# Optimization experiments

Measured on AMD Instinct MI355X. Metric: run time of the kernel, lower is better.

Reference implementation:

```python
import jax, jax.numpy as jnp
import numpy as np

D_MODEL = 768
N_HEADS = 12
HEAD_DIM = D_MODEL // N_HEADS


def setup_inputs() -> dict:
    key = jax.random.key(0)
    k_x, k_wqkv, k_bqkv, k_wp, k_bp = jax.random.split(key, 5)
    s = 1.0 / np.sqrt(D_MODEL)
    return {
        "x": jax.random.normal(k_x, (8, 1024, D_MODEL), dtype=jnp.float32),
        "w_qkv": jax.random.uniform(k_wqkv, (D_MODEL, 3 * D_MODEL), jnp.float32, -s, s),
        "b_qkv": jax.random.uniform(k_bqkv, (3 * D_MODEL,), jnp.float32, -s, s),
        "w_proj": jax.random.uniform(k_wp, (D_MODEL, D_MODEL), jnp.float32, -s, s),
        "b_proj": jax.random.uniform(k_bp, (D_MODEL,), jnp.float32, -s, s),
    }


def reference(x, w_qkv, b_qkv, w_proj, b_proj):
    # x: [B, N, D]. Dropout is identity in eval mode.
    B, N, D = x.shape
    qkv = x @ w_qkv + b_qkv  # [B, N, 3D]
    qkv = qkv.reshape(B, N, 3, N_HEADS, HEAD_DIM).transpose(2, 0, 3, 1, 4)
    q, k, v = qkv[0], qkv[1], qkv[2]  # each [B, H, N, hd]
    scale = 1.0 / np.sqrt(HEAD_DIM).astype(np.float32)
    attn = jnp.einsum("bhqd,bhkd->bhqk", q, k) * scale  # [B, H, N, N]
    attn = jax.nn.softmax(attn, axis=-1)
    out = jnp.einsum("bhqk,bhkd->bhqd", attn, v)  # [B, H, N, hd]
    out = out.transpose(0, 2, 1, 3).reshape(B, N, D)
    return out @ w_proj + b_proj
```

## Files before the change

kernel.cpp:

```cpp
#include <hip/hip_runtime.h>
#include <math.h>

#define D_MODEL 768
#define NHEADS  12
#define HDIM    64
#define SEQ     1024
#define BATCH   8
#define NBH     (BATCH*NHEADS)
#define M_TOTAL (BATCH*SEQ)
#define KT_D    (D_MODEL/32)
#define QKV_COLS (3*D_MODEL)

typedef __attribute__((ext_vector_type(8))) short bf16x8;
typedef __attribute__((ext_vector_type(4))) float f32x4;

#define MFMA16(a,b,c) __builtin_amdgcn_mfma_f32_16x16x32_bf16((a),(b),(c),0,0,0)

#define QSCALE 0.18033688011112042f

__device__ inline unsigned short f2bf(float f) {
    unsigned u = __float_as_uint(f);
    u += 0x7FFFu + ((u >> 16) & 1u);
    return (unsigned short)(u >> 16);
}
__device__ inline void gload16(const void* g, const void* l) {
    __builtin_amdgcn_global_load_lds(
        (const __attribute__((address_space(1))) unsigned*)g,
        (__attribute__((address_space(3))) unsigned*)l, 16, 0, 0);
}
__device__ inline float exp2_fast(float x) {
#if __has_builtin(__builtin_amdgcn_exp2f)
    return __builtin_amdgcn_exp2f(x);
#else
    float r; asm("v_exp_f32 %0, %1" : "=v"(r) : "v"(x)); return r;
#endif
}


#define NA_TOT 786432
#define NB1_TOT 221184
#define NB2_TOT 73728

__global__ __launch_bounds__(256)
void convert_all(const float* __restrict__ x,    unsigned short* __restrict__ Xf,
                 const float* __restrict__ wq,   unsigned short* __restrict__ Wq,
                 const float* __restrict__ wp,   unsigned short* __restrict__ Wp)
{
    const int gid = blockIdx.x * 256 + threadIdx.x;
    const int lane = gid & 63;
    if (gid < NA_TOT) {
        const int sub = gid >> 6;
        const int kt = sub % KT_D;
        const int mt = sub / KT_D;
        const float* s = x + (size_t)(mt*16 + (lane & 15)) * D_MODEL + kt*32 + (lane >> 4)*8;
        float4 v0 = *(const float4*)(s);
        float4 v1 = *(const float4*)(s + 4);
        float vv[8] = {v0.x, v0.y, v0.z, v0.w, v1.x, v1.y, v1.z, v1.w};
        union { unsigned short u[8]; bf16x8 v; } H;
        #pragma unroll
        for (int i = 0; i < 8; ++i) H.u[i] = f2bf(vv[i]);
        *(bf16x8*)(Xf + (size_t)sub * 512 + lane * 8) = H.v;
    } else {
        const float* src;
        unsigned short* dst;
        int sub, ldN;
        if (gid < NA_TOT + NB1_TOT) {
            src = wq; dst = Wq; ldN = QKV_COLS; sub = (gid - NA_TOT) >> 6;
        } else if (gid < NA_TOT + NB1_TOT + NB2_TOT) {
            src = wp; dst = Wp; ldN = D_MODEL; sub = (gid - NA_TOT - NB1_TOT) >> 6;
        } else {
            return;
        }
        const int kt = sub % KT_D;
        const int nt = sub / KT_D;
        const int n  = nt*16 + (lane & 15);
        const int k0 = kt*32 + (lane >> 4)*8;
        const float* s = src + (size_t)k0 * ldN + n;
        union { unsigned short u[8]; bf16x8 v; } H;
        #pragma unroll
        for (int i = 0; i < 8; ++i) H.u[i] = f2bf(s[(size_t)i * ldN]);
        *(bf16x8*)(dst + (size_t)sub * 512 + lane * 8) = H.v;
    }
}

template<int MODE>
__global__ __launch_bounds__(MODE == 0 ? 512 : 256, 4)
void gemm_frag(const unsigned short* __restrict__ Af,
               const unsigned short* __restrict__ Bf,
               const float* __restrict__ bias,
               float* __restrict__ outF,
               unsigned short* __restrict__ outQ,
               unsigned short* __restrict__ outK,
               unsigned short* __restrict__ outV)
{
    constexpr int NW     = (MODE == 0) ? 8 : 4;
    constexpr int NSUB_N = (MODE == 0) ? 8 : 4;
    constexpr int ACH    = 8;
    constexpr int NCH    = ACH + NSUB_N;
    constexpr int CPW    = NCH / NW;
    __shared__ unsigned short sm[3][NCH * 512];
    const int t = threadIdx.x, lane = t & 63, wid = t >> 6;
    const int wr = (MODE == 0) ? (wid >> 2) : (wid >> 1);
    const int wc = (MODE == 0) ? (wid & 3)  : (wid & 1);
    const int bid = blockIdx.x;
    const int mb = (bid & 7) * 8 + ((bid >> 3) & 7);
    const int nb = bid >> 6;

    f32x4 acc[4][2] = {};

    auto stageTo = [&](unsigned short* Lb, int ktv) {
        #pragma unroll
        for (int i = 0; i < CPW; ++i) {
            const int c = wid * CPW + i;
            const unsigned short* g;
            if (c < ACH) {
                g = Af + ((size_t)(mb*8 + c)*KT_D + ktv)*512 + lane*8;
            } else {
                const int j = c - ACH;
                g = Bf + ((size_t)(nb*NSUB_N + j)*KT_D + ktv)*512 + lane*8;
            }
            gload16(g, (const char*)Lb + (size_t)c*1024);
        }
    };
    auto waitCPW = [&] {
        if (MODE == 0) asm volatile("s_waitcnt vmcnt(2)" ::: "memory");
        else           asm volatile("s_waitcnt vmcnt(3)" ::: "memory");
    };
    auto compute = [&](const unsigned short* Lb) {
        bf16x8 bh[2];
        #pragma unroll
        for (int n = 0; n < 2; ++n)
            bh[n] = *(const bf16x8*)(Lb + (ACH + wc*2 + n)*512 + lane*8);
        bf16x8 ah[4];
        #pragma unroll
        for (int m = 0; m < 4; ++m)
            ah[m] = *(const bf16x8*)(Lb + (wr*4 + m)*512 + lane*8);
        __builtin_amdgcn_s_setprio(1);
        #pragma unroll
        for (int m = 0; m < 4; ++m)
            #pragma unroll
            for (int n = 0; n < 2; ++n)
                acc[m][n] = MFMA16(ah[m], bh[n], acc[m][n]);
        __builtin_amdgcn_s_setprio(0);
    };

    stageTo(&sm[0][0], 0);
    stageTo(&sm[1][0], 1);

    for (int ktb = 0; ktb < KT_D - 3; ktb += 3) {
        waitCPW(); __builtin_amdgcn_s_barrier();
        stageTo(&sm[2][0], ktb + 2);  compute(&sm[0][0]);
        waitCPW(); __builtin_amdgcn_s_barrier();
        stageTo(&sm[0][0], ktb + 3);  compute(&sm[1][0]);
        waitCPW(); __builtin_amdgcn_s_barrier();
        stageTo(&sm[1][0], ktb + 4);  compute(&sm[2][0]);
    }
    waitCPW(); __builtin_amdgcn_s_barrier();
    stageTo(&sm[2][0], KT_D - 1);  compute(&sm[0][0]);
    waitCPW(); __builtin_amdgcn_s_barrier();
    compute(&sm[1][0]);
    asm volatile("s_waitcnt vmcnt(0)" ::: "memory");
    __builtin_amdgcn_s_barrier();
    compute(&sm[2][0]);

    const int rowW = mb*128 + wr*64;
    const int colW = nb*(NSUB_N*16) + wc*32;
    if (MODE == 1) {
        #pragma unroll
        for (int m = 0; m < 4; ++m)
            #pragma unroll
            for (int n = 0; n < 2; ++n) {
                const int col = colW + n*16 + (lane & 15);
                const float bv = bias[col];
                #pragma unroll
                for (int r = 0; r < 4; ++r) {
                    const int row = rowW + m*16 + (lane >> 4)*4 + r;
                    outF[(size_t)row * D_MODEL + col] = acc[m][n][r] + bv;
                }
            }
    } else {
        const int which = colW / D_MODEL;
        const int h     = (colW % D_MODEL) >> 6;
        #pragma unroll
        for (int m = 0; m < 4; ++m)
            #pragma unroll
            for (int n = 0; n < 2; ++n) {
                const int col = colW + n*16 + (lane & 15);
                const int d = col & 63;
                const float bv = bias[col];
                #pragma unroll
                for (int r = 0; r < 4; ++r) {
                    const int row = rowW + m*16 + (lane >> 4)*4 + r;
                    const int b = row >> 10, sq = row & 1023;
                    float val = acc[m][n][r] + bv;
                    if (which <= 1) {
                        if (which == 0) val *= QSCALE;
                        const int sub = (sq >> 4)*2 + (d >> 5);
                        const int lp  = (sq & 15) + (((d & 31) >> 3) << 4);
                        unsigned short* dst = (which == 0) ? outQ : outK;
                        dst[(size_t)(b*NHEADS + h)*65536
                            + (size_t)sub*512 + lp*8 + (d & 7)] = f2bf(val);
                    } else {
                        const int sub = (d >> 4)*32 + (sq >> 5);
                        const int lp  = (d & 15) + (((sq & 31) >> 3) << 4);
                        outV[(size_t)(b*NHEADS + h)*65536
                             + (size_t)sub*512 + lp*8 + (sq & 7)] = f2bf(val);
                    }
                }
            }
    }
}

__global__ __launch_bounds__(512, 6)
void attn_frag(const unsigned short* __restrict__ Qf,
               const unsigned short* __restrict__ Kf,
               const unsigned short* __restrict__ Vf,
               unsigned short* __restrict__ Cf)
{
    __shared__ unsigned short Ksm[2][8 * 512];
    __shared__ unsigned short Vsm[2][8 * 512];
    __shared__ unsigned short Psm[8 * 1024];

    const int t = threadIdx.x, lane = t & 63, wid = t >> 6;
    const int bid = blockIdx.x;
    const int qb  = (bid >> 3) & 7;
    const int bh  = (bid & 7) * 12 + (bid >> 6);
    const int mt0 = qb*8 + wid;
    const size_t kBase = (size_t)bh * 65536;

    const int slot  = lane & 7;
    const int colg  = (lane & 15) >> 3;
    const int qrow0 = (lane >> 4) * 4;

    auto stage = [&](int b, int jt) {
        #pragma unroll
        for (int i = 0; i < 2; ++i) {
            const int ch = wid*2 + i;
            if (ch < 8) {
                const unsigned short* gk = Kf + kBase + (size_t)(jt*8 + ch)*512;
                gload16(gk + lane*8, (const char*)&Ksm[b][0] + (size_t)ch*1024);
            } else {
                const int cv = ch - 8;
                const unsigned short* gv = Vf + kBase
                    + (size_t)((cv >> 1)*32 + jt*2 + (cv & 1))*512;
                gload16(gv + lane*8, (const char*)&Vsm[b][0] + (size_t)cv*1024);
            }
        }
    };

    stage(0, 0);

    bf16x8 qh[2];
    #pragma unroll
    for (int kt = 0; kt < 2; ++kt)
        qh[kt] = *(const bf16x8*)(Qf + kBase + ((size_t)mt0*2 + kt)*512 + lane*8);

    bf16x8 ones;
    #pragma unroll
    for (int i = 0; i < 8; ++i) ones[i] = (short)0x3F80;

    f32x4 out[4] = {};
    f32x4 lacc = {};
    float m_run[4];
    #pragma unroll
    for (int r = 0; r < 4; ++r) m_run[r] = -INFINITY;

    unsigned short* Pw = Psm + wid * 1024;

    __syncthreads();

    for (int jt = 0; jt < 16; ++jt) {
        const int cur = jt & 1;
        if (jt + 1 < 16) stage(cur ^ 1, jt + 1);

        f32x4 s[4] = {};
        __builtin_amdgcn_s_setprio(1);
        #pragma unroll
        for (int jn = 0; jn < 4; ++jn)
            #pragma unroll
            for (int kt = 0; kt < 2; ++kt) {
                const bf16x8 kh = *(const bf16x8*)(&Ksm[cur][0] + (jn*2 + kt)*512 + lane*8);
                s[jn] = MFMA16(qh[kt], kh, s[jn]);
            }
        __builtin_amdgcn_s_setprio(0);

        float mx[4];
        int ok = 1;
        #pragma unroll
        for (int r = 0; r < 4; ++r) {
            const float v = fmaxf(fmaxf(s[0][r], s[1][r]), fmaxf(s[2][r], s[3][r]));
            mx[r] = v;
            ok &= (v <= m_run[r] + 8.0f);
        }
        if (!__all(ok)) {
            float alf[4];
            #pragma unroll
            for (int r = 0; r < 4; ++r) {
                float v = mx[r];
                #pragma unroll
                for (int msk = 1; msk < 16; msk <<= 1)
                    v = fmaxf(v, __shfl_xor(v, msk));
                const float mn = fmaxf(m_run[r], v);
                alf[r] = exp2_fast(m_run[r] - mn);
                m_run[r] = mn;
            }
            #pragma unroll
            for (int dt = 0; dt < 4; ++dt)
                #pragma unroll
                for (int r = 0; r < 4; ++r)
                    out[dt][r] *= alf[r];
            #pragma unroll
            for (int r = 0; r < 4; ++r)
                lacc[r] *= alf[r];
        }

        #pragma unroll
        for (int r = 0; r < 4; ++r) {
            const float mb_ = m_run[r];
            const int tl   = qrow0 + r + (colg << 4);
            const int idxb = ((tl << 3) | slot) ^ (tl & 0x18);
            #pragma unroll
            for (int jn = 0; jn < 4; ++jn) {
                const float e = exp2_fast(s[jn][r] - mb_);
                Pw[(jn >> 1)*512 + idxb + ((jn & 1) << 8)]
                    = (unsigned short)(__float_as_uint(e) >> 16);
            }
        }

        const int rdswz = (lane*8) ^ (lane & 0x18);
        __builtin_amdgcn_s_setprio(1);
        #pragma unroll
        for (int kt2 = 0; kt2 < 2; ++kt2) {
            const bf16x8 pa = *(const bf16x8*)(Pw + kt2*512 + rdswz);
            #pragma unroll
            for (int dt = 0; dt < 4; ++dt) {
                const bf16x8 vh = *(const bf16x8*)(&Vsm[cur][0] + (dt*2 + kt2)*512 + lane*8);
                out[dt] = MFMA16(pa, vh, out[dt]);
            }
            lacc = MFMA16(pa, ones, lacc);
        }
        __builtin_amdgcn_s_setprio(0);

        __syncthreads();
    }

    const int b = bh / NHEADS, h = bh % NHEADS;
    #pragma unroll
    for (int r = 0; r < 4; ++r) {
        const float inv = 1.0f / lacc[r];
        const int sq = mt0*16 + qrow0 + r;
        const int mrow = b*SEQ + sq;
        #pragma unroll
        for (int dt = 0; dt < 4; ++dt) {
            const int c = h*64 + dt*16 + (lane & 15);
            const float val = out[dt][r] * inv;
            Cf[((size_t)(mrow >> 4)*KT_D + (c >> 5))*512
               + ((mrow & 15) + (((c & 31) >> 3) << 4))*8 + (c & 7)] = f2bf(val);
        }
    }
}

extern "C" void kernel_launch(void* const* d_in, const int* in_sizes, int n_in,
                              void* d_out, int out_size, void* d_ws, size_t ws_size,
                              hipStream_t stream)
{
    const float* x      = (const float*)d_in[0];
    const float* w_qkv  = (const float*)d_in[1];
    const float* b_qkv  = (const float*)d_in[2];
    const float* w_proj = (const float*)d_in[3];
    const float* b_proj = (const float*)d_in[4];
    float* out = (float*)d_out;

    unsigned short* ws = (unsigned short*)d_ws;
    unsigned short* Xf = ws;
    unsigned short* Wq = Xf + 6291456;
    unsigned short* Wp = Wq + 1769472;
    unsigned short* Qf = Wp + 589824;
    unsigned short* Kf = Qf + 6291456;
    unsigned short* Vf = Kf + 6291456;
    unsigned short* Cf = Vf + 6291456;

    convert_all<<<dim3(4224), 256, 0, stream>>>(x, Xf, w_qkv, Wq, w_proj, Wp);

    gemm_frag<0><<<dim3(1152), 512, 0, stream>>>(Xf, Wq, b_qkv, nullptr, Qf, Kf, Vf);
    attn_frag<<<dim3(768), 512, 0, stream>>>(Qf, Kf, Vf, Cf);
    gemm_frag<1><<<dim3(768), 256, 0, stream>>>(Cf, Wp, b_proj, out,
                                                nullptr, nullptr, nullptr);
}
```

Measured before the change: 112.3 us.

## Compute transposed S tile so each lane owns one query row

New measurement: 107.1 us, median of 2. 1.05x faster.

```diff
diff --git a/kernel.cpp b/kernel.cpp
--- a/kernel.cpp
+++ b/kernel.cpp
@@ -228,9 +228,8 @@
     const int mt0 = qb*8 + wid;
     const size_t kBase = (size_t)bh * 65536;
 
-    const int slot  = lane & 7;
-    const int colg  = (lane & 15) >> 3;
     const int qrow0 = (lane >> 4) * 4;
+    const int slot0 = ((lane >> 4) & 1) * 4;
 
     auto stage = [&](int b, int jt) {
         #pragma unroll
@@ -261,9 +260,7 @@
 
     f32x4 out[4] = {};
     f32x4 lacc = {};
-    float m_run[4];
-    #pragma unroll
-    for (int r = 0; r < 4; ++r) m_run[r] = -INFINITY;
+    float m_run = -INFINITY;
 
     unsigned short* Pw = Psm + wid * 1024;
 
@@ -280,51 +277,45 @@
             #pragma unroll
             for (int kt = 0; kt < 2; ++kt) {
                 const bf16x8 kh = *(const bf16x8*)(&Ksm[cur][0] + (jn*2 + kt)*512 + lane*8);
-                s[jn] = MFMA16(qh[kt], kh, s[jn]);
+                s[jn] = MFMA16(kh, qh[kt], s[jn]);
             }
         __builtin_amdgcn_s_setprio(0);
 
-        float mx[4];
-        int ok = 1;
-        #pragma unroll
-        for (int r = 0; r < 4; ++r) {
-            const float v = fmaxf(fmaxf(s[0][r], s[1][r]), fmaxf(s[2][r], s[3][r]));
-            mx[r] = v;
-            ok &= (v <= m_run[r] + 8.0f);
-        }
-        if (!__all(ok)) {
-            float alf[4];
+        float mymax = s[0][0];
+        #pragma unroll
+        for (int jn = 0; jn < 4; ++jn)
+            #pragma unroll
+            for (int r = 0; r < 4; ++r)
+                mymax = fmaxf(mymax, s[jn][r]);
+        if (!__all(mymax <= m_run + 8.0f)) {
+            float v = mymax;
+            v = fmaxf(v, __shfl_xor(v, 16));
+            v = fmaxf(v, __shfl_xor(v, 32));
+            const float mn = fmaxf(m_run, v);
+            const float al = exp2_fast(m_run - mn);
+            m_run = mn;
             #pragma unroll
             for (int r = 0; r < 4; ++r) {
-                float v = mx[r];
+                const float alf = __shfl(al, qrow0 + r);
                 #pragma unroll
-                for (int msk = 1; msk < 16; msk <<= 1)
-                    v = fmaxf(v, __shfl_xor(v, msk));
-                const float mn = fmaxf(m_run[r], v);
-                alf[r] = exp2_fast(m_run[r] - mn);
-                m_run[r] = mn;
-            }
-            #pragma unroll
-            for (int dt = 0; dt < 4; ++dt)
-                #pragma unroll
-                for (int r = 0; r < 4; ++r)
-                    out[dt][r] *= alf[r];
-            #pragma unroll
-            for (int r = 0; r < 4; ++r)
-                lacc[r] *= alf[r];
-        }
-
-        #pragma unroll
-        for (int r = 0; r < 4; ++r) {
-            const float mb_ = m_run[r];
-            const int tl   = qrow0 + r + (colg << 4);
-            const int idxb = ((tl << 3) | slot) ^ (tl & 0x18);
-            #pragma unroll
-            for (int jn = 0; jn < 4; ++jn) {
-                const float e = exp2_fast(s[jn][r] - mb_);
-                Pw[(jn >> 1)*512 + idxb + ((jn & 1) << 8)]
-                    = (unsigned short)(__float_as_uint(e) >> 16);
-            }
+                for (int dt = 0; dt < 4; ++dt)
+                    out[dt][r] *= alf;
+                lacc[r] *= alf;
+            }
+        }
+
+        #pragma unroll
+        for (int jn = 0; jn < 4; ++jn) {
+            const unsigned b0 = __float_as_uint(exp2_fast(s[jn][0] - m_run));
+            const unsigned b1 = __float_as_uint(exp2_fast(s[jn][1] - m_run));
+            const unsigned b2 = __float_as_uint(exp2_fast(s[jn][2] - m_run));
+            const unsigned b3 = __float_as_uint(exp2_fast(s[jn][3] - m_run));
+            const unsigned u0 = (b0 >> 16) | (b1 & 0xFFFF0000u);
+            const unsigned u1 = (b2 >> 16) | (b3 & 0xFFFF0000u);
+            const int hi2 = ((jn & 1) << 1) + (lane >> 5);
+            const int lp  = (lane & 15) + (hi2 << 4);
+            const int idx = (((lp << 3) | slot0) ^ (lp & 0x18));
+            *(uint2*)&Pw[(jn >> 1)*512 + idx] = make_uint2(u0, u1);
         }
 
         const int rdswz = (lane*8) ^ (lane & 0x18);
```
